# Kernel optimization log

Hardware: AMD Instinct MI355X
Metric: run time of the kernel (lower is better)

Reference implementation:

```python
import jax, jax.numpy as jnp
import numpy as np

B, S, D, H, DFF = 4, 2048, 1024, 16, 4096
HD = D // H  # head_dim = 64


def rmsnorm(x, scale, eps=1e-6):
    var = jnp.mean(jnp.square(x), axis=-1, keepdims=True)
    return x * jax.lax.rsqrt(var + eps) * scale


def setup_inputs() -> dict:
    key = jax.random.key(0)
    ks = jax.random.split(key, 16)
    s = 1.0 / np.sqrt(D)
    inp = {
        "x": jax.random.normal(ks[0], (B, S, D), jnp.float32),
        "wq": jax.random.normal(ks[1], (D, D), jnp.float32) * s,
        "bq": jnp.zeros((D,), jnp.float32),
        "wk": jax.random.normal(ks[2], (D, D), jnp.float32) * s,
        "bk": jnp.zeros((D,), jnp.float32),
        "wv": jax.random.normal(ks[3], (D, D), jnp.float32) * s,
        "bv": jnp.zeros((D,), jnp.float32),
        "wbeta": jax.random.normal(ks[4], (D, H), jnp.float32) * s,
        "bbeta": jnp.zeros((H,), jnp.float32),
        "wo": jax.random.normal(ks[5], (D, D), jnp.float32) * s,
        "bo": jnp.zeros((D,), jnp.float32),
        "w1": jax.random.normal(ks[6], (D, DFF), jnp.float32) * s,
        "b1": jnp.zeros((DFF,), jnp.float32),
        "w2": jax.random.normal(ks[7], (DFF, D), jnp.float32) * (1.0 / np.sqrt(DFF)),
        "b2": jnp.zeros((D,), jnp.float32),
        "ln1_scale": jnp.ones((D,), jnp.float32),
        "ln2_scale": jnp.ones((D,), jnp.float32),
    }
    return inp


def gdn_attention(x, wq, bq, wk, bk, wv, bv, wbeta, bbeta, wo, bo):
    b, s, _ = x.shape
    q = (x @ wq + bq).reshape(b, s, H, HD)
    k = (x @ wk + bk).reshape(b, s, H, HD)
    v = (x @ wv + bv).reshape(b, s, H, HD)
    k = k / (jnp.linalg.norm(k, axis=-1, keepdims=True) + 1e-6)
    beta = jax.nn.sigmoid(x @ wbeta + bbeta)[..., None]  # (b, s, H, 1)

    # time-major for scan: (s, b, H, ...)
    q = jnp.transpose(q, (1, 0, 2, 3))
    k = jnp.transpose(k, (1, 0, 2, 3))
    v = jnp.transpose(v, (1, 0, 2, 3))
    beta = jnp.transpose(beta, (1, 0, 2, 3))

    def _step(Sm, inputs):
        q_t, k_t, v_t, beta_t = inputs
        Sk = jnp.einsum('bhde,bhe->bhd', Sm, k_t)
        delta = v_t - Sk
        Sm = Sm + beta_t[..., None] * jnp.einsum('bhd,bhe->bhde', delta, k_t)
        o_t = jnp.einsum('bhde,bhe->bhd', Sm, q_t)
        return Sm, o_t

    S0 = jnp.zeros((b, H, HD, HD), x.dtype)
    _, outputs = jax.lax.scan(_step, S0, (q, k, v, beta))
    outputs = jnp.transpose(outputs, (1, 0, 2, 3)).reshape(b, s, D)
    return outputs @ wo + bo


def reference(x, wq, bq, wk, bk, wv, bv, wbeta, bbeta, wo, bo,
              w1, b1, w2, b2, ln1_scale, ln2_scale):
    residual = x
    h = rmsnorm(x, ln1_scale)
    h = gdn_attention(h, wq, bq, wk, bk, wv, bv, wbeta, bbeta, wo, bo)
    x = h + residual
    residual = x
    h = rmsnorm(x, ln2_scale)
    h = jax.nn.gelu(h @ w1 + b1) @ w2 + b2
    return h + residual
```

## Files before the change

### kernel.cpp

```cpp
#include <hip/hip_runtime.h>

#define DEV __device__ __forceinline__

typedef short bf16x8 __attribute__((ext_vector_type(8)));
typedef float f32x4 __attribute__((ext_vector_type(4)));
typedef unsigned int uint;

#define SBAR()   asm volatile("s_barrier" ::: "memory")
#define WAITV(n) asm volatile("s_waitcnt vmcnt(" #n ")" ::: "memory")
#define WAITL()  asm volatile("s_waitcnt lgkmcnt(0)" ::: "memory")

DEV unsigned short f2b(float f) {
    uint u = __float_as_uint(f);
    u += 0x7fffu + ((u >> 16) & 1u);
    return (unsigned short)(u >> 16);
}
DEV uint packbf2(float a, float b) { return (uint)f2b(a) | ((uint)f2b(b) << 16); }
DEV float b2f(unsigned short s) { return __uint_as_float(((uint)s) << 16); }
DEV float b2f_lo(uint u) { return __uint_as_float(u << 16); }
DEV float b2f_hi(uint u) { return __uint_as_float(u & 0xffff0000u); }

DEV void async_cp16(const void* g, void* l) {
    __builtin_amdgcn_global_load_lds(
        (const __attribute__((address_space(1))) unsigned int*)g,
        (__attribute__((address_space(3))) unsigned int*)l, 16, 0, 0);
}

DEV float quad_sum(float x) {
    x += __int_as_float(__builtin_amdgcn_update_dpp(0, __float_as_int(x), 0xB1, 0xF, 0xF, true));
    x += __int_as_float(__builtin_amdgcn_update_dpp(0, __float_as_int(x), 0x4E, 0xF, 0xF, true));
    return x;
}

DEV float gelu_f(float u) {
    float p = u + 0.044715f * u * u * u;
    float e = __expf(-1.5957691216f * p);
    return __fdividef(u, 1.f + e);
}

DEV void dec8(uint4 p, float* o) {
    o[0] = b2f_lo(p.x); o[1] = b2f_hi(p.x); o[2] = b2f_lo(p.y); o[3] = b2f_hi(p.y);
    o[4] = b2f_lo(p.z); o[5] = b2f_hi(p.z); o[6] = b2f_lo(p.w); o[7] = b2f_hi(p.w);
}

__global__ __launch_bounds__(256) void weight_prep_k(
    const float* __restrict__ wq, const float* __restrict__ wk,
    const float* __restrict__ wv, const float* __restrict__ wbeta,
    const float* __restrict__ wo, const float* __restrict__ w1,
    const float* __restrict__ w2,
    unsigned short* __restrict__ wqkvT, unsigned short* __restrict__ woT,
    unsigned short* __restrict__ w1T, unsigned short* __restrict__ w2T,
    const float* __restrict__ bq, const float* __restrict__ bk,
    const float* __restrict__ bv, const float* __restrict__ bb,
    float* __restrict__ biasc)
{
    const int id = blockIdx.x;
    if (id >= 12544) {
        int i = (id - 12544) * 256 + threadIdx.x;
        if (i >= 3328) return;
        float v = 0.f;
        if (i < 1024)      v = bq[i];
        else if (i < 2048) v = bk[i - 1024];
        else if (i < 3072) v = bv[i - 2048];
        else if (i < 3088) v = bb[i - 3072];
        biasc[i] = v;
        return;
    }
    const float* in; unsigned short* out; int K, N, KT, loc;
    if (id < 1024)      { in = wq;    out = wqkvT;               K = 1024; N = 1024; KT = 32;  loc = id; }
    else if (id < 2048) { in = wk;    out = wqkvT + 1024 * 1024; K = 1024; N = 1024; KT = 32;  loc = id - 1024; }
    else if (id < 3072) { in = wv;    out = wqkvT + 2048 * 1024; K = 1024; N = 1024; KT = 32;  loc = id - 2048; }
    else if (id < 3328) { in = wbeta; out = wqkvT + 3072 * 1024; K = 1024; N = 16;   KT = 32;  loc = id - 3072; }
    else if (id < 4352) { in = wo;    out = woT;                 K = 1024; N = 1024; KT = 32;  loc = id - 3328; }
    else if (id < 8448) { in = w1;    out = w1T;                 K = 1024; N = 4096; KT = 32;  loc = id - 4352; }
    else                { in = w2;    out = w2T;                 K = 4096; N = 1024; KT = 128; loc = id - 8448; }
    const int k0 = (loc % KT) * 32, n0 = (loc / KT) * 32;

    __shared__ float tile[32][33];
    const int tx = threadIdx.x & 31, ty = threadIdx.x >> 5;
#pragma unroll
    for (int i = 0; i < 32; i += 8) {
        int n = n0 + tx;
        tile[ty + i][tx] = (n < N) ? in[(size_t)(k0 + ty + i) * N + n] : 0.0f;
    }
    __syncthreads();
#pragma unroll
    for (int i = 0; i < 32; i += 8) {
        out[(size_t)(n0 + ty + i) * K + (k0 + tx)] = f2b(tile[tx][ty + i]);
    }
}

__global__ __launch_bounds__(256) void rmsnorm_cast_k(
    const float* __restrict__ x, const float* __restrict__ scale,
    unsigned short* __restrict__ out)
{
    const int row = blockIdx.x;
    const int t = threadIdx.x;
    const float4 v = *(const float4*)(x + (size_t)row * 1024 + t * 4);
    float ss = v.x * v.x + v.y * v.y + v.z * v.z + v.w * v.w;
#pragma unroll
    for (int off = 1; off < 64; off <<= 1) ss += __shfl_xor(ss, off);
    __shared__ float wsum[4];
    if ((t & 63) == 0) wsum[t >> 6] = ss;
    __syncthreads();
    const float tot = wsum[0] + wsum[1] + wsum[2] + wsum[3];
    const float inv = rsqrtf(tot * (1.0f / 1024.0f) + 1e-6f);
    const float4 sc = *(const float4*)(scale + t * 4);
    uint lo = (uint)f2b(v.x * inv * sc.x) | ((uint)f2b(v.y * inv * sc.y) << 16);
    uint hi = (uint)f2b(v.z * inv * sc.z) | ((uint)f2b(v.w * inv * sc.w) << 16);
    uint2 pkd; pkd.x = lo; pkd.y = hi;
    *(uint2*)(out + (size_t)row * 1024 + t * 4) = pkd;
}

template <bool GELU, bool GUARD>
__global__ __launch_bounds__(512, 2) void gemm256(
    const unsigned short* __restrict__ A, const unsigned short* __restrict__ BT,
    const float* __restrict__ bias, unsigned short* __restrict__ C,
    int Nstride, int Nreal, int K)
{
    __shared__ __align__(16) unsigned short As[4][256 * 32];
    __shared__ __align__(16) unsigned short Bs[4][256 * 32];
    const int tid = threadIdx.x;
    const int wid = tid >> 6;
    const int lane = tid & 63;
    const int l16 = lane & 15, quad = lane >> 4;
    const int wm = wid & 1, wn = wid >> 1;
    const int m0 = blockIdx.x << 8, n0 = blockIdx.y << 8;

    const int srow = (wid << 5) + (lane >> 2);
    const int scol = ((lane & 3) ^ ((lane >> 3) & 3)) << 3;
    const unsigned short* Ag = A + (size_t)(m0 + srow) * K + scol;
    const unsigned short* Bg = BT + (size_t)(n0 + srow) * K + scol;
    const size_t rstep16 = (size_t)16 * K;
    const int ldst = wid << 10;

    f32x4 acc[8][4];
#pragma unroll
    for (int i = 0; i < 8; i++)
#pragma unroll
        for (int j = 0; j < 4; j++) acc[i][j] = (f32x4)0.f;

    const int ksw = (quad ^ ((l16 >> 1) & 3)) << 3;
    const int aoff = ((wm << 7) + l16) * 32 + ksw;
    const int boff = ((wn << 6) + l16) * 32 + ksw;

    const int nt = K >> 5;
    async_cp16(Ag, &As[0][ldst]);
    async_cp16(Ag + rstep16, &As[0][ldst + 512]);
    async_cp16(Bg, &Bs[0][ldst]);
    async_cp16(Bg + rstep16, &Bs[0][ldst + 512]);
    async_cp16(Ag + 32, &As[1][ldst]);
    async_cp16(Ag + 32 + rstep16, &As[1][ldst + 512]);
    async_cp16(Bg + 32, &Bs[1][ldst]);
    async_cp16(Bg + 32 + rstep16, &Bs[1][ldst + 512]);
    WAITV(4);
    SBAR();

    for (int tb = 0; tb < nt; tb += 4) {
#pragma unroll
        for (int u = 0; u < 4; ++u) {
            const int t = tb + u;
            const int pb = (u + 2) & 3;
            const bool st = (t + 2) < nt;
            const size_t kpre = (size_t)(t + 2) << 5;
            bf16x8 af[8], bfr[4];
#pragma unroll
            for (int mi = 0; mi < 8; mi++) af[mi] = *(const bf16x8*)&As[u][aoff + mi * 512];
#pragma unroll
            for (int ni = 0; ni < 4; ni++) bfr[ni] = *(const bf16x8*)&Bs[u][boff + ni * 512];
            if (st) {
                async_cp16(Ag + kpre, &As[pb][ldst]);
                async_cp16(Ag + kpre + rstep16, &As[pb][ldst + 512]);
                async_cp16(Bg + kpre, &Bs[pb][ldst]);
                async_cp16(Bg + kpre + rstep16, &Bs[pb][ldst + 512]);
                WAITV(4);
            } else {
                WAITV(0);
            }
            SBAR();
            __builtin_amdgcn_s_setprio(1);
#pragma unroll
            for (int mi = 0; mi < 8; mi++)
#pragma unroll
                for (int ni = 0; ni < 4; ni++)
                    acc[mi][ni] = __builtin_amdgcn_mfma_f32_16x16x32_bf16(af[mi], bfr[ni], acc[mi][ni], 0, 0, 0);
            __builtin_amdgcn_s_setprio(0);
            SBAR();
        }
    }

    float bv[4];
    const int ccol = n0 + (wn << 6) + l16;
#pragma unroll
    for (int ni = 0; ni < 4; ni++) bv[ni] = bias[ccol + ni * 16];
#pragma unroll
    for (int mi = 0; mi < 8; mi++) {
        const int row = m0 + (wm << 7) + mi * 16 + (quad << 2);
#pragma unroll
        for (int r = 0; r < 4; r++) {
            unsigned short* Crow = C + (size_t)(row + r) * Nstride + ccol;
#pragma unroll
            for (int ni = 0; ni < 4; ni++) {
                float v = acc[mi][ni][r] + bv[ni];
                if (GELU) v = gelu_f(v);
                if (!GUARD || (ccol + ni * 16) < Nreal) Crow[ni * 16] = f2b(v);
            }
        }
    }
}

template <bool ADD>
__global__ __launch_bounds__(512, 2) void gemm128n256(
    const unsigned short* __restrict__ A, const unsigned short* __restrict__ BT,
    const float* __restrict__ bias, const float* __restrict__ add,
    float* __restrict__ C, int N, int K)
{
    __shared__ __align__(16) unsigned short As[4][128 * 32];
    __shared__ __align__(16) unsigned short Bs[4][256 * 32];
    const int tid = threadIdx.x;
    const int wid = tid >> 6;
    const int lane = tid & 63;
    const int l16 = lane & 15, quad = lane >> 4;
    const int wm = wid & 1, wn = wid >> 1;
    const int m0 = blockIdx.x << 7, n0 = blockIdx.y << 8;

    const int arow = (wid << 4) + (lane >> 2);
    const int brow = (wid << 5) + (lane >> 2);
    const int scol = ((lane & 3) ^ ((lane >> 3) & 3)) << 3;
    const unsigned short* Ag = A + (size_t)(m0 + arow) * K + scol;
    const unsigned short* Bg = BT + (size_t)(n0 + brow) * K + scol;
    const size_t rstep16 = (size_t)16 * K;
    const int lda = wid << 9;
    const int ldb = wid << 10;

    f32x4 acc[4][4];
#pragma unroll
    for (int i = 0; i < 4; i++)
#pragma unroll
        for (int j = 0; j < 4; j++) acc[i][j] = (f32x4)0.f;

    const int ksw = (quad ^ ((l16 >> 1) & 3)) << 3;
    const int aoff = ((wm << 6) + l16) * 32 + ksw;
    const int boff = ((wn << 6) + l16) * 32 + ksw;

    const int nt = K >> 5;
    async_cp16(Ag, &As[0][lda]);
    async_cp16(Bg, &Bs[0][ldb]);
    async_cp16(Bg + rstep16, &Bs[0][ldb + 512]);
    async_cp16(Ag + 32, &As[1][lda]);
    async_cp16(Bg + 32, &Bs[1][ldb]);
    async_cp16(Bg + 32 + rstep16, &Bs[1][ldb + 512]);
    WAITV(3);
    SBAR();

    for (int tb = 0; tb < nt; tb += 4) {
#pragma unroll
        for (int u = 0; u < 4; ++u) {
            const int t = tb + u;
            const int pb = (u + 2) & 3;
            const bool st = (t + 2) < nt;
            const size_t kpre = (size_t)(t + 2) << 5;
            bf16x8 af[4], bfr[4];
#pragma unroll
            for (int mi = 0; mi < 4; mi++) af[mi] = *(const bf16x8*)&As[u][aoff + mi * 512];
#pragma unroll
            for (int ni = 0; ni < 4; ni++) bfr[ni] = *(const bf16x8*)&Bs[u][boff + ni * 512];
            if (st) {
                async_cp16(Ag + kpre, &As[pb][lda]);
                async_cp16(Bg + kpre, &Bs[pb][ldb]);
                async_cp16(Bg + kpre + rstep16, &Bs[pb][ldb + 512]);
                WAITV(3);
            } else {
                WAITV(0);
            }
            SBAR();
            __builtin_amdgcn_s_setprio(1);
#pragma unroll
            for (int mi = 0; mi < 4; mi++)
#pragma unroll
                for (int ni = 0; ni < 4; ni++)
                    acc[mi][ni] = __builtin_amdgcn_mfma_f32_16x16x32_bf16(af[mi], bfr[ni], acc[mi][ni], 0, 0, 0);
            __builtin_amdgcn_s_setprio(0);
            SBAR();
        }
    }

    const int ccol = n0 + (wn << 6) + l16;
    float bv[4];
#pragma unroll
    for (int ni = 0; ni < 4; ni++) bv[ni] = bias[ccol + ni * 16];
#pragma unroll
    for (int mi = 0; mi < 4; mi++) {
        const int row = m0 + (wm << 6) + mi * 16 + (quad << 2);
#pragma unroll
        for (int r = 0; r < 4; r++) {
#pragma unroll
            for (int ni = 0; ni < 4; ni++) {
                size_t idx = (size_t)(row + r) * N + ccol + ni * 16;
                float v = acc[mi][ni][r] + bv[ni];
                if (ADD) v += add[idx];
                C[idx] = v;
            }
        }
    }
}


__global__ __launch_bounds__(256) void gdn_prep(
    unsigned short* __restrict__ qkv, unsigned short* __restrict__ Wg,
    unsigned short* __restrict__ ZTg, unsigned short* __restrict__ KTg)
{
    const int chunk = blockIdx.x, bh = blockIdx.y;
    const int b = bh >> 4, h = bh & 15;
    __shared__ float Ks[64 * 68];
    __shared__ float Ws[64 * 65];
    __shared__ float Zs[64 * 65];
    __shared__ float Asl[64 * 65];
    __shared__ float bs[64];
    const int tid = threadIdx.x;
    const int t = tid >> 2, c = tid & 3;
    unsigned short* rowp = qkv + (size_t)(b * 2048 + chunk * 64 + t) * 3200;

    float kn[16];
    {
        uint4 ka = *(const uint4*)(rowp + 1024 + h * 64 + 16 * c);
        uint4 kb = *(const uint4*)(rowp + 1024 + h * 64 + 16 * c + 8);
        dec8(ka, kn); dec8(kb, kn + 8);
    }
    float ss = 0.f;
#pragma unroll
    for (int j = 0; j < 16; j++) ss += kn[j] * kn[j];
    ss = quad_sum(ss);
    const float inv = 1.f / (sqrtf(ss) + 1e-6f);
#pragma unroll
    for (int j = 0; j < 16; j++) kn[j] *= inv;
#pragma unroll
    for (int j = 0; j < 16; j++) Ks[t * 68 + 16 * c + j] = kn[j];
    {
        uint4 p0, p1;
        p0.x = packbf2(kn[0], kn[1]);  p0.y = packbf2(kn[2], kn[3]);
        p0.z = packbf2(kn[4], kn[5]);  p0.w = packbf2(kn[6], kn[7]);
        p1.x = packbf2(kn[8], kn[9]);  p1.y = packbf2(kn[10], kn[11]);
        p1.z = packbf2(kn[12], kn[13]); p1.w = packbf2(kn[14], kn[15]);
        *(uint4*)(rowp + 1024 + h * 64 + 16 * c) = p0;
        *(uint4*)(rowp + 1024 + h * 64 + 16 * c + 8) = p1;
    }
    if (c == 0) bs[t] = 1.f / (1.f + __expf(-b2f(rowp[3072 + h])));
    __syncthreads();

    const float beta = bs[t];
#pragma unroll
    for (int j = 0; j < 16; j++) Ws[t * 65 + 16 * c + j] = beta * kn[j];
    {
        float vv[16];
        uint4 va = *(const uint4*)(rowp + 2048 + h * 64 + 16 * c);
        uint4 vb = *(const uint4*)(rowp + 2048 + h * 64 + 16 * c + 8);
        dec8(va, vv); dec8(vb, vv + 8);
#pragma unroll
        for (int j = 0; j < 16; j++) Zs[t * 65 + 16 * c + j] = beta * vv[j];
    }
    __syncthreads();

    {
        const int tt = tid >> 4, sx = tid & 15;
        float dm[4][4];
#pragma unroll
        for (int i = 0; i < 4; i++)
#pragma unroll
            for (int j = 0; j < 4; j++) dm[i][j] = 0.f;
        for (int d = 0; d < 64; d++) {
            float kt[4], ksv[4];
#pragma unroll
            for (int i = 0; i < 4; i++) kt[i] = Ks[(4 * tt + i) * 68 + d];
#pragma unroll
            for (int j = 0; j < 4; j++) ksv[j] = Ks[(4 * sx + j) * 68 + d];
#pragma unroll
            for (int i = 0; i < 4; i++)
#pragma unroll
                for (int j = 0; j < 4; j++) dm[i][j] += kt[i] * ksv[j];
        }
#pragma unroll
        for (int i = 0; i < 4; i++)
#pragma unroll
            for (int j = 0; j < 4; j++) {
                int T = 4 * tt + i, S_ = 4 * sx + j;
                Asl[T * 65 + S_] = (S_ < T) ? bs[T] * dm[i][j] : 0.f;
            }
    }
    __syncthreads();

    {
        const int wid = tid >> 6, lane = tid & 63;
        for (int qi = 0; qi < 4; qi++) {
            if (qi > 0) {
                const int tb = qi * 16 + wid * 4;
                float aw[4], az[4];
#pragma unroll
                for (int i = 0; i < 4; i++) { aw[i] = Ws[(tb + i) * 65 + lane]; az[i] = Zs[(tb + i) * 65 + lane]; }
                for (int s = 0; s < qi * 16; s++) {
                    float wsv = Ws[s * 65 + lane], zsv = Zs[s * 65 + lane];
#pragma unroll
                    for (int i = 0; i < 4; i++) {
                        float a = Asl[(tb + i) * 65 + s];
                        aw[i] -= a * wsv; az[i] -= a * zsv;
                    }
                }
#pragma unroll
                for (int i = 0; i < 4; i++) { Ws[(tb + i) * 65 + lane] = aw[i]; Zs[(tb + i) * 65 + lane] = az[i]; }
            }
            __syncthreads();
            if (wid == 0) {
                for (int T = qi * 16; T < qi * 16 + 16; T++) {
                    float a_ = Ws[T * 65 + lane];
                    for (int s = qi * 16; s < T; s++) a_ -= Asl[T * 65 + s] * Ws[s * 65 + lane];
                    Ws[T * 65 + lane] = a_;
                }
            } else if (wid == 1) {
                for (int T = qi * 16; T < qi * 16 + 16; T++) {
                    float a_ = Zs[T * 65 + lane];
                    for (int s = qi * 16; s < T; s++) a_ -= Asl[T * 65 + s] * Zs[s * 65 + lane];
                    Zs[T * 65 + lane] = a_;
                }
            }
            __syncthreads();
        }
    }

    const size_t cbase = ((size_t)bh * 32 + chunk) * 4096;
    {
#pragma unroll
        for (int half = 0; half < 2; half++) {
            uint4 w4;
            w4.x = packbf2(Ws[t * 65 + 16 * c + half * 8 + 0], Ws[t * 65 + 16 * c + half * 8 + 1]);
            w4.y = packbf2(Ws[t * 65 + 16 * c + half * 8 + 2], Ws[t * 65 + 16 * c + half * 8 + 3]);
            w4.z = packbf2(Ws[t * 65 + 16 * c + half * 8 + 4], Ws[t * 65 + 16 * c + half * 8 + 5]);
            w4.w = packbf2(Ws[t * 65 + 16 * c + half * 8 + 6], Ws[t * 65 + 16 * c + half * 8 + 7]);
            *(uint4*)(Wg + cbase + (size_t)((2 * c + half) * 64 + t) * 8) = w4;
        }
    }
    {
        const int jj = tid >> 2, tq = tid & 3;
#pragma unroll
        for (int half = 0; half < 2; half++) {
            uint4 z4;
            int i0 = half * 8;
            z4.x = packbf2(Zs[(16 * tq + i0 + 0) * 65 + jj], Zs[(16 * tq + i0 + 1) * 65 + jj]);
            z4.y = packbf2(Zs[(16 * tq + i0 + 2) * 65 + jj], Zs[(16 * tq + i0 + 3) * 65 + jj]);
            z4.z = packbf2(Zs[(16 * tq + i0 + 4) * 65 + jj], Zs[(16 * tq + i0 + 5) * 65 + jj]);
            z4.w = packbf2(Zs[(16 * tq + i0 + 6) * 65 + jj], Zs[(16 * tq + i0 + 7) * 65 + jj]);
            *(uint4*)(ZTg + cbase + (size_t)((2 * tq + half) * 64 + jj) * 8) = z4;
        }
    }
    {
        const int dd = tid >> 2, tq = tid & 3;
#pragma unroll
        for (int half = 0; half < 2; half++) {
            uint4 k4;
            int i0 = half * 8;
            k4.x = packbf2(Ks[(16 * tq + i0 + 0) * 68 + dd], Ks[(16 * tq + i0 + 1) * 68 + dd]);
            k4.y = packbf2(Ks[(16 * tq + i0 + 2) * 68 + dd], Ks[(16 * tq + i0 + 3) * 68 + dd]);
            k4.z = packbf2(Ks[(16 * tq + i0 + 4) * 68 + dd], Ks[(16 * tq + i0 + 5) * 68 + dd]);
            k4.w = packbf2(Ks[(16 * tq + i0 + 6) * 68 + dd], Ks[(16 * tq + i0 + 7) * 68 + dd]);
            *(uint4*)(KTg + cbase + (size_t)((2 * tq + half) * 64 + dd) * 8) = k4;
        }
    }
}

__global__ __launch_bounds__(64, 1) void gdn_prop_mfma(
    const unsigned short* __restrict__ Wg, const unsigned short* __restrict__ KTg,
    const unsigned short* __restrict__ ZTg, unsigned short* __restrict__ Sg,
    unsigned short* __restrict__ YTg)
{
    const int bh = blockIdx.x;
    const int jb = blockIdx.y << 4;
    __shared__ unsigned short Wb[2][4096];
    __shared__ unsigned short KTb[2][4096];
    __shared__ unsigned short ZTb[2][1024];
    __shared__ unsigned short Sb[1024];
    const int lane = threadIdx.x;
    const int l16 = lane & 15, quad = lane >> 4;

    f32x4 Sacc[4];
#pragma unroll
    for (int dt = 0; dt < 4; dt++) Sacc[dt] = (f32x4)0.f;

    {
        const size_t cb0 = ((size_t)bh * 32) * 4096;
#pragma unroll
        for (int p = 0; p < 8; p++) async_cp16(Wg + cb0 + p * 512 + lane * 8, &Wb[0][p * 512]);
#pragma unroll
        for (int p = 0; p < 8; p++) async_cp16(KTg + cb0 + p * 512 + lane * 8, &KTb[0][p * 512]);
#pragma unroll
        for (int c = 0; c < 2; c++)
            async_cp16(ZTg + cb0 + (size_t)((c * 4 + (lane >> 4)) * 64 + jb + (lane & 15)) * 8,
                       &ZTb[0][c * 512]);
    }
    WAITV(0);

    for (int ch = 0; ch < 32; ch++) {
        const int cur = ch & 1, nxt = cur ^ 1;
        const size_t cbase = ((size_t)bh * 32 + ch) * 4096;

        if (ch + 1 < 32) {
            const size_t cbn = cbase + 4096;
#pragma unroll
            for (int p = 0; p < 8; p++) async_cp16(Wg + cbn + p * 512 + lane * 8, &Wb[nxt][p * 512]);
#pragma unroll
            for (int p = 0; p < 8; p++) async_cp16(KTg + cbn + p * 512 + lane * 8, &KTb[nxt][p * 512]);
#pragma unroll
            for (int c = 0; c < 2; c++)
                async_cp16(ZTg + cbn + (size_t)((c * 4 + (lane >> 4)) * 64 + jb + (lane & 15)) * 8,
                           &ZTb[nxt][c * 512]);
        }

#pragma unroll
        for (int dt = 0; dt < 4; dt++) {
#pragma unroll
            for (int r = 0; r < 4; r++) {
                const int lj = quad * 4 + r;
                Sb[((2 * dt + (l16 >> 3)) * 16 + lj) * 8 + (l16 & 7)] = f2b(Sacc[dt][r]);
            }
        }
        {
            const int gd = lane >> 3, lj0 = (lane & 7) * 2;
            uint4 s0 = *(const uint4*)&Sb[lane * 16];
            uint4 s1 = *(const uint4*)&Sb[lane * 16 + 8];
            *(uint4*)(Sg + cbase + (size_t)(gd * 64 + jb + lj0) * 8) = s0;
            *(uint4*)(Sg + cbase + (size_t)(gd * 64 + jb + lj0 + 1) * 8) = s1;
        }

        f32x4 t1[4];
#pragma unroll
        for (int tt = 0; tt < 4; tt++) t1[tt] = (f32x4)0.f;
#pragma unroll
        for (int kh = 0; kh < 2; kh++) {
            const int g = kh * 4 + quad;
            bf16x8 afr = *(const bf16x8*)&Sb[(g * 16 + l16) * 8];
#pragma unroll
            for (int tt = 0; tt < 4; tt++) {
                bf16x8 bfr = *(const bf16x8*)&Wb[cur][(g * 64 + tt * 16 + l16) * 8];
                t1[tt] = __builtin_amdgcn_mfma_f32_16x16x32_bf16(afr, bfr, t1[tt], 0, 0, 0);
            }
        }
#pragma unroll
        for (int tt = 0; tt < 4; tt++) {
            const int t = tt * 16 + l16;
            unsigned short ybf[4];
#pragma unroll
            for (int r = 0; r < 4; r++) {
                const int lj = quad * 4 + r;
                const float z = b2f(ZTb[cur][((t >> 3) * 16 + lj) * 8 + (t & 7)]);
                ybf[r] = f2b(z - t1[tt][r]);
            }
#pragma unroll
            for (int r = 0; r < 4; r++) {
                const int lj = quad * 4 + r;
                ZTb[cur][((t >> 3) * 16 + lj) * 8 + (t & 7)] = ybf[r];
            }
        }
#pragma unroll
        for (int kh = 0; kh < 2; kh++) {
            const int g = kh * 4 + quad;
            bf16x8 afr = *(const bf16x8*)&ZTb[cur][(g * 16 + l16) * 8];
#pragma unroll
            for (int dt = 0; dt < 4; dt++) {
                bf16x8 bfr = *(const bf16x8*)&KTb[cur][(g * 64 + dt * 16 + l16) * 8];
                Sacc[dt] = __builtin_amdgcn_mfma_f32_16x16x32_bf16(afr, bfr, Sacc[dt], 0, 0, 0);
            }
        }
        {
            const int gt = lane >> 3, lj0 = (lane & 7) * 2;
            uint4 y0 = *(const uint4*)&ZTb[cur][lane * 16];
            uint4 y1 = *(const uint4*)&ZTb[cur][lane * 16 + 8];
            *(uint4*)(YTg + cbase + (size_t)(gt * 64 + jb + lj0) * 8) = y0;
            *(uint4*)(YTg + cbase + (size_t)(gt * 64 + jb + lj0 + 1) * 8) = y1;
        }
        WAITV(0);
    }
}

__global__ __launch_bounds__(256) void gdn_out(
    const unsigned short* __restrict__ qkv, const unsigned short* __restrict__ YTg,
    const unsigned short* __restrict__ Sg, unsigned short* __restrict__ attn)
{
    const int chunk = blockIdx.x, bh = blockIdx.y;
    const int b = bh >> 4, h = bh & 15;
    __shared__ unsigned short QbU[8 * 516];
    __shared__ unsigned short KbU[8 * 516];
    __shared__ unsigned short StU[8 * 516];
    __shared__ unsigned short YtU[8 * 516];
    __shared__ unsigned short MhU[8 * 516];
    __shared__ unsigned short MlU[8 * 516];
    const int tid = threadIdx.x;
    const int wid = tid >> 6, lane = tid & 63;
    const int l16 = lane & 15, quad = lane >> 4;
    const size_t cbase = ((size_t)bh * 32 + chunk) * 4096;

    {
        const int t = tid >> 2, c = tid & 3;
        const unsigned short* rowp = qkv + (size_t)(b * 2048 + chunk * 64 + t) * 3200;
        uint4 qa = *(const uint4*)(rowp + h * 64 + 16 * c);
        uint4 qb = *(const uint4*)(rowp + h * 64 + 16 * c + 8);
        uint4 ka = *(const uint4*)(rowp + 1024 + h * 64 + 16 * c);
        uint4 kb = *(const uint4*)(rowp + 1024 + h * 64 + 16 * c + 8);
        *(uint4*)&QbU[(2 * c) * 516 + t * 8]     = qa;
        *(uint4*)&QbU[(2 * c + 1) * 516 + t * 8] = qb;
        *(uint4*)&KbU[(2 * c) * 516 + t * 8]     = ka;
        *(uint4*)&KbU[(2 * c + 1) * 516 + t * 8] = kb;
        const int g = tid >> 5, row = (tid * 2) & 63;
        uint4 s0 = *(const uint4*)(Sg + cbase + tid * 16);
        uint4 s1 = *(const uint4*)(Sg + cbase + tid * 16 + 8);
        *(uint4*)&StU[g * 516 + row * 8]       = s0;
        *(uint4*)&StU[g * 516 + (row + 1) * 8] = s1;
        uint4 y0 = *(const uint4*)(YTg + cbase + tid * 16);
        uint4 y1 = *(const uint4*)(YTg + cbase + tid * 16 + 8);
        *(uint4*)&YtU[g * 516 + row * 8]       = y0;
        *(uint4*)&YtU[g * 516 + (row + 1) * 8] = y1;
    }
    __syncthreads();

    f32x4 m[4], o[4];
#pragma unroll
    for (int i = 0; i < 4; i++) { m[i] = (f32x4)0.f; o[i] = (f32x4)0.f; }

#pragma unroll
    for (int kh = 0; kh < 2; kh++) {
        const int g = kh * 4 + quad;
        bf16x8 afr = *(const bf16x8*)&QbU[g * 516 + (wid * 16 + l16) * 8];
#pragma unroll
        for (int st = 0; st < 4; st++) {
            bf16x8 bk = *(const bf16x8*)&KbU[g * 516 + (st * 16 + l16) * 8];
            m[st] = __builtin_amdgcn_mfma_f32_16x16x32_bf16(afr, bk, m[st], 0, 0, 0);
        }
#pragma unroll
        for (int jt = 0; jt < 4; jt++) {
            bf16x8 bs_ = *(const bf16x8*)&StU[g * 516 + (jt * 16 + l16) * 8];
            o[jt] = __builtin_amdgcn_mfma_f32_16x16x32_bf16(afr, bs_, o[jt], 0, 0, 0);
        }
    }

#pragma unroll
    for (int st = 0; st < 4; st++) {
#pragma unroll
        for (int r = 0; r < 4; r++) {
            const int t = wid * 16 + quad * 4 + r;
            const int s = st * 16 + l16;
            float v = (s <= t) ? m[st][r] : 0.f;
            unsigned short hi = f2b(v);
            unsigned short lo = f2b(v - b2f(hi));
            const int addr = (s >> 3) * 516 + t * 8 + (s & 7);
            MhU[addr] = hi;
            MlU[addr] = lo;
        }
    }
    __syncthreads();

#pragma unroll
    for (int kh = 0; kh < 2; kh++) {
        const int g = kh * 4 + quad;
        bf16x8 ah = *(const bf16x8*)&MhU[g * 516 + (wid * 16 + l16) * 8];
        bf16x8 al = *(const bf16x8*)&MlU[g * 516 + (wid * 16 + l16) * 8];
#pragma unroll
        for (int jt = 0; jt < 4; jt++) {
            bf16x8 by = *(const bf16x8*)&YtU[g * 516 + (jt * 16 + l16) * 8];
            o[jt] = __builtin_amdgcn_mfma_f32_16x16x32_bf16(ah, by, o[jt], 0, 0, 0);
            o[jt] = __builtin_amdgcn_mfma_f32_16x16x32_bf16(al, by, o[jt], 0, 0, 0);
        }
    }

#pragma unroll
    for (int jt = 0; jt < 4; jt++) {
#pragma unroll
        for (int r = 0; r < 4; r++) {
            const int t = wid * 16 + quad * 4 + r;
            attn[(size_t)(b * 2048 + chunk * 64 + t) * 1024 + h * 64 + jt * 16 + l16] = f2b(o[jt][r]);
        }
    }
}

static constexpr size_t OFF_H     = 0;
static constexpr size_t OFF_WQKVT = OFF_H + 16777216;
static constexpr size_t OFF_WOT   = OFF_WQKVT + 6553600;
static constexpr size_t OFF_W1T   = OFF_WOT + 2097152;
static constexpr size_t OFF_W2T   = OFF_W1T + 8388608;
static constexpr size_t OFF_BIAS  = OFF_W2T + 8388608;
static constexpr size_t OFF_QKV   = OFF_BIAS + 16384;
static constexpr size_t OFF_ATTN  = OFF_QKV + 67108864;
static constexpr size_t OFF_Y1    = OFF_ATTN + 16777216;
static constexpr size_t OFF_WG    = OFF_Y1 + 33554432;
static constexpr size_t OFF_YG    = OFF_WG + 16777216;

extern "C" void kernel_launch(void* const* d_in, const int* in_sizes, int n_in,
                              void* d_out, int out_size, void* d_ws, size_t ws_size,
                              hipStream_t stream)
{
    const float* x     = (const float*)d_in[0];
    const float* wq    = (const float*)d_in[1];
    const float* bq    = (const float*)d_in[2];
    const float* wk    = (const float*)d_in[3];
    const float* bk    = (const float*)d_in[4];
    const float* wv    = (const float*)d_in[5];
    const float* bv    = (const float*)d_in[6];
    const float* wbeta = (const float*)d_in[7];
    const float* bbeta = (const float*)d_in[8];
    const float* wo    = (const float*)d_in[9];
    const float* bo    = (const float*)d_in[10];
    const float* w1    = (const float*)d_in[11];
    const float* b1    = (const float*)d_in[12];
    const float* w2    = (const float*)d_in[13];
    const float* b2    = (const float*)d_in[14];
    const float* ln1   = (const float*)d_in[15];
    const float* ln2   = (const float*)d_in[16];

    char* ws = (char*)d_ws;
    unsigned short* hbuf  = (unsigned short*)(ws + OFF_H);
    unsigned short* Sg    = (unsigned short*)(ws + OFF_H);
    unsigned short* wqkvT = (unsigned short*)(ws + OFF_WG);
    unsigned short* woT   = (unsigned short*)(ws + OFF_WOT);
    unsigned short* w1T   = (unsigned short*)(ws + OFF_W1T);
    unsigned short* w2T   = (unsigned short*)(ws + OFF_W2T);
    float*          biasc = (float*)(ws + OFF_BIAS);
    unsigned short* qkvU  = (unsigned short*)(ws + OFF_QKV);
    unsigned short* gbuf  = (unsigned short*)(ws + OFF_QKV);
    unsigned short* attn  = (unsigned short*)(ws + OFF_ATTN);
    float*          y1    = (float*)(ws + OFF_Y1);
    unsigned short* ZTg   = (unsigned short*)(ws + OFF_Y1);
    unsigned short* KTg   = (unsigned short*)(ws + OFF_Y1 + 16777216);
    unsigned short* Wg    = (unsigned short*)(ws + OFF_WG);
    unsigned short* YTg   = (unsigned short*)(ws + OFF_YG);
    float*          out   = (float*)d_out;

    weight_prep_k<<<12557, 256, 0, stream>>>(wq, wk, wv, wbeta, wo, w1, w2,
                                             wqkvT, woT, w1T, w2T,
                                             bq, bk, bv, bbeta, biasc);

    rmsnorm_cast_k<<<8192, 256, 0, stream>>>(x, ln1, hbuf);
    gemm256<false, true><<<dim3(32, 13), 512, 0, stream>>>(hbuf, wqkvT, biasc, qkvU, 3200, 3200, 1024);
    gdn_prep<<<dim3(32, 64), 256, 0, stream>>>(qkvU, Wg, ZTg, KTg);
    gdn_prop_mfma<<<dim3(64, 4), 64, 0, stream>>>(Wg, KTg, ZTg, Sg, YTg);
    gdn_out<<<dim3(32, 64), 256, 0, stream>>>(qkvU, YTg, Sg, attn);
    gemm128n256<true><<<dim3(64, 4), 512, 0, stream>>>(attn, woT, bo, x, y1, 1024, 1024);
    rmsnorm_cast_k<<<8192, 256, 0, stream>>>(y1, ln2, hbuf);
    gemm256<true, false><<<dim3(32, 16), 512, 0, stream>>>(hbuf, w1T, b1, gbuf, 4096, 4096, 1024);
    gemm128n256<true><<<dim3(64, 4), 512, 0, stream>>>(gbuf, w2T, b2, y1, out, 1024, 4096);
}
```

Baseline: 576.2 us.

## Restructure gemm256 to BK=64 double-buffered pipeline and use MFMA for chunk K·Kᵀ

The main 256x256 GEMM moves from four 32-wide K stages to two 64-wide K buffers. It interleaves A-fragment loads, async global-to-LDS staging and MFMA phases inside each iteration, and uses a new 8-way XOR swizzle. This is meant to cut barriers per K element and hide load latency better. In gdn_prep, the scalar FP32 64x64 K·Kᵀ product is replaced by bf16 MFMA from a transposed bf16 copy of K kept in LDS, which lowers precision on the strictly lower-triangular A matrix. The second GEMM's shared arrays are only renamed.

```diff
diff --git a/kernel.cpp b/kernel.cpp
--- a/kernel.cpp
+++ b/kernel.cpp
@@ -112,14 +112,44 @@
     *(uint2*)(out + (size_t)row * 1024 + t * 4) = pkd;
 }
 
+#define STG(dst, srcp, half, kt)                                                       \
+    do {                                                                               \
+        async_cp16(srcp + (size_t)((half) * 128) * K + ((kt) << 6),                    \
+                   dst + ((half) * 128) * 64 + lds);                                   \
+        async_cp16(srcp + (size_t)((half) * 128 + 64) * K + ((kt) << 6),               \
+                   dst + ((half) * 128 + 64) * 64 + lds);                              \
+    } while (0)
+
+#define LD_A(MI0)                                                                      \
+    do {                                                                               \
+        af[0] = *(const bf16x8*)&Ab[arow0 + (MI0) * 1024 + k0];                        \
+        af[1] = *(const bf16x8*)&Ab[arow0 + (MI0) * 1024 + k1];                        \
+        af[2] = *(const bf16x8*)&Ab[arow0 + ((MI0) + 1) * 1024 + k0];                  \
+        af[3] = *(const bf16x8*)&Ab[arow0 + ((MI0) + 1) * 1024 + k1];                  \
+    } while (0)
+
+#define PH_MFMA(MI0)                                                                   \
+    do {                                                                               \
+        __builtin_amdgcn_s_setprio(1);                                                 \
+        _Pragma("unroll")                                                              \
+        for (int kh = 0; kh < 2; kh++)                                                 \
+            _Pragma("unroll")                                                          \
+            for (int m = 0; m < 2; m++)                                                \
+                _Pragma("unroll")                                                      \
+                for (int ni = 0; ni < 4; ni++)                                         \
+                    acc[(MI0) + m][ni] = __builtin_amdgcn_mfma_f32_16x16x32_bf16(      \
+                        af[m * 2 + kh], bf[ni * 2 + kh], acc[(MI0) + m][ni], 0, 0, 0); \
+        __builtin_amdgcn_s_setprio(0);                                                 \
+    } while (0)
+
 template <bool GELU, bool GUARD>
 __global__ __launch_bounds__(512, 2) void gemm256(
     const unsigned short* __restrict__ A, const unsigned short* __restrict__ BT,
     const float* __restrict__ bias, unsigned short* __restrict__ C,
     int Nstride, int Nreal, int K)
 {
-    __shared__ __align__(16) unsigned short As[4][256 * 32];
-    __shared__ __align__(16) unsigned short Bs[4][256 * 32];
+    __shared__ __align__(16) unsigned short As[2][256 * 64];
+    __shared__ __align__(16) unsigned short Bs[2][256 * 64];
     const int tid = threadIdx.x;
     const int wid = tid >> 6;
     const int lane = tid & 63;
@@ -127,12 +157,11 @@
     const int wm = wid & 1, wn = wid >> 1;
     const int m0 = blockIdx.x << 8, n0 = blockIdx.y << 8;
 
-    const int srow = (wid << 5) + (lane >> 2);
-    const int scol = ((lane & 3) ^ ((lane >> 3) & 3)) << 3;
+    const int srow = (wid << 3) + (lane >> 3);
+    const int scol = ((lane & 7) ^ ((lane >> 3) & 7)) << 3;
     const unsigned short* Ag = A + (size_t)(m0 + srow) * K + scol;
     const unsigned short* Bg = BT + (size_t)(n0 + srow) * K + scol;
-    const size_t rstep16 = (size_t)16 * K;
-    const int ldst = wid << 10;
+    const int lds = (wid << 3) * 64;
 
     f32x4 acc[8][4];
 #pragma unroll
@@ -140,53 +169,43 @@
 #pragma unroll
         for (int j = 0; j < 4; j++) acc[i][j] = (f32x4)0.f;
 
-    const int ksw = (quad ^ ((l16 >> 1) & 3)) << 3;
-    const int aoff = ((wm << 7) + l16) * 32 + ksw;
-    const int boff = ((wn << 6) + l16) * 32 + ksw;
-
-    const int nt = K >> 5;
-    async_cp16(Ag, &As[0][ldst]);
-    async_cp16(Ag + rstep16, &As[0][ldst + 512]);
-    async_cp16(Bg, &Bs[0][ldst]);
-    async_cp16(Bg + rstep16, &Bs[0][ldst + 512]);
-    async_cp16(Ag + 32, &As[1][ldst]);
-    async_cp16(Ag + 32 + rstep16, &As[1][ldst + 512]);
-    async_cp16(Bg + 32, &Bs[1][ldst]);
-    async_cp16(Bg + 32 + rstep16, &Bs[1][ldst + 512]);
-    WAITV(4);
-    SBAR();
-
-    for (int tb = 0; tb < nt; tb += 4) {
-#pragma unroll
-        for (int u = 0; u < 4; ++u) {
-            const int t = tb + u;
-            const int pb = (u + 2) & 3;
-            const bool st = (t + 2) < nt;
-            const size_t kpre = (size_t)(t + 2) << 5;
-            bf16x8 af[8], bfr[4];
-#pragma unroll
-            for (int mi = 0; mi < 8; mi++) af[mi] = *(const bf16x8*)&As[u][aoff + mi * 512];
-#pragma unroll
-            for (int ni = 0; ni < 4; ni++) bfr[ni] = *(const bf16x8*)&Bs[u][boff + ni * 512];
-            if (st) {
-                async_cp16(Ag + kpre, &As[pb][ldst]);
-                async_cp16(Ag + kpre + rstep16, &As[pb][ldst + 512]);
-                async_cp16(Bg + kpre, &Bs[pb][ldst]);
-                async_cp16(Bg + kpre + rstep16, &Bs[pb][ldst + 512]);
-                WAITV(4);
-            } else {
-                WAITV(0);
-            }
-            SBAR();
-            __builtin_amdgcn_s_setprio(1);
-#pragma unroll
-            for (int mi = 0; mi < 8; mi++)
-#pragma unroll
-                for (int ni = 0; ni < 4; ni++)
-                    acc[mi][ni] = __builtin_amdgcn_mfma_f32_16x16x32_bf16(af[mi], bfr[ni], acc[mi][ni], 0, 0, 0);
-            __builtin_amdgcn_s_setprio(0);
-            SBAR();
-        }
+    const int arow0 = ((wm << 7) + l16) << 6;
+    const int brow0 = ((wn << 6) + l16) << 6;
+    const int k0 = (quad ^ (l16 & 7)) << 3;
+    const int k1 = k0 ^ 32;
+
+    const int nt = K >> 6;
+    STG(Bs[0], Bg, 0, 0); STG(Bs[0], Bg, 1, 0);
+    STG(As[0], Ag, 0, 0); STG(As[0], Ag, 1, 0);
+    STG(Bs[1], Bg, 0, 1); STG(Bs[1], Bg, 1, 1);
+
+    for (int t = 0; t < nt; ++t) {
+        const unsigned short* Ab = As[t & 1];
+        const unsigned short* Bb = Bs[t & 1];
+        unsigned short* An = As[(t + 1) & 1];
+        unsigned short* Bn = Bs[t & 1];
+        const bool s1 = (t + 1) < nt, s2 = (t + 2) < nt;
+        if (s2) { WAITV(4); } else { WAITV(0); }
+        SBAR();
+        bf16x8 af[4], bf[8];
+#pragma unroll
+        for (int ni = 0; ni < 4; ni++) {
+            bf[ni * 2]     = *(const bf16x8*)&Bb[brow0 + ni * 1024 + k0];
+            bf[ni * 2 + 1] = *(const bf16x8*)&Bb[brow0 + ni * 1024 + k1];
+        }
+        LD_A(0);
+        if (s1) { STG(An, Ag, 0, t + 1); }
+        PH_MFMA(0);
+        LD_A(2);
+        if (s1) { STG(An, Ag, 1, t + 1); }
+        PH_MFMA(2);
+        SBAR();
+        LD_A(4);
+        if (s2) { STG(Bn, Bg, 0, t + 2); }
+        PH_MFMA(4);
+        LD_A(6);
+        if (s2) { STG(Bn, Bg, 1, t + 2); }
+        PH_MFMA(6);
     }
 
     float bv[4];
@@ -215,8 +234,8 @@
     const float* __restrict__ bias, const float* __restrict__ add,
     float* __restrict__ C, int N, int K)
 {
-    __shared__ __align__(16) unsigned short As[4][128 * 32];
-    __shared__ __align__(16) unsigned short Bs[4][256 * 32];
+    __shared__ __align__(16) unsigned short As2[4][128 * 32];
+    __shared__ __align__(16) unsigned short Bs2[4][256 * 32];
     const int tid = threadIdx.x;
     const int wid = tid >> 6;
     const int lane = tid & 63;
@@ -244,12 +263,12 @@
     const int boff = ((wn << 6) + l16) * 32 + ksw;
 
     const int nt = K >> 5;
-    async_cp16(Ag, &As[0][lda]);
-    async_cp16(Bg, &Bs[0][ldb]);
-    async_cp16(Bg + rstep16, &Bs[0][ldb + 512]);
-    async_cp16(Ag + 32, &As[1][lda]);
-    async_cp16(Bg + 32, &Bs[1][ldb]);
-    async_cp16(Bg + 32 + rstep16, &Bs[1][ldb + 512]);
+    async_cp16(Ag, &As2[0][lda]);
+    async_cp16(Bg, &Bs2[0][ldb]);
+    async_cp16(Bg + rstep16, &Bs2[0][ldb + 512]);
+    async_cp16(Ag + 32, &As2[1][lda]);
+    async_cp16(Bg + 32, &Bs2[1][ldb]);
+    async_cp16(Bg + 32 + rstep16, &Bs2[1][ldb + 512]);
     WAITV(3);
     SBAR();
 
@@ -262,13 +281,13 @@
             const size_t kpre = (size_t)(t + 2) << 5;
             bf16x8 af[4], bfr[4];
 #pragma unroll
-            for (int mi = 0; mi < 4; mi++) af[mi] = *(const bf16x8*)&As[u][aoff + mi * 512];
-#pragma unroll
-            for (int ni = 0; ni < 4; ni++) bfr[ni] = *(const bf16x8*)&Bs[u][boff + ni * 512];
+            for (int mi = 0; mi < 4; mi++) af[mi] = *(const bf16x8*)&As2[u][aoff + mi * 512];
+#pragma unroll
+            for (int ni = 0; ni < 4; ni++) bfr[ni] = *(const bf16x8*)&Bs2[u][boff + ni * 512];
             if (st) {
-                async_cp16(Ag + kpre, &As[pb][lda]);
-                async_cp16(Bg + kpre, &Bs[pb][ldb]);
-                async_cp16(Bg + kpre + rstep16, &Bs[pb][ldb + 512]);
+                async_cp16(Ag + kpre, &As2[pb][lda]);
+                async_cp16(Bg + kpre, &Bs2[pb][ldb]);
+                async_cp16(Bg + kpre + rstep16, &Bs2[pb][ldb + 512]);
                 WAITV(3);
             } else {
                 WAITV(0);
@@ -317,6 +336,7 @@
     __shared__ float Zs[64 * 65];
     __shared__ float Asl[64 * 65];
     __shared__ float bs[64];
+    __shared__ __align__(16) unsigned short KTb[4096];
     const int tid = threadIdx.x;
     const int t = tid >> 2, c = tid & 3;
     unsigned short* rowp = qkv + (size_t)(b * 2048 + chunk * 64 + t) * 3200;
@@ -344,6 +364,8 @@
         p1.z = packbf2(kn[12], kn[13]); p1.w = packbf2(kn[14], kn[15]);
         *(uint4*)(rowp + 1024 + h * 64 + 16 * c) = p0;
         *(uint4*)(rowp + 1024 + h * 64 + 16 * c + 8) = p1;
+        *(uint4*)&KTb[((2 * c) * 64 + t) * 8]     = p0;
+        *(uint4*)&KTb[((2 * c + 1) * 64 + t) * 8] = p1;
     }
     if (c == 0) bs[t] = 1.f / (1.f + __expf(-b2f(rowp[3072 + h])));
     __syncthreads();
@@ -362,29 +384,28 @@
     __syncthreads();
 
     {
-        const int tt = tid >> 4, sx = tid & 15;
-        float dm[4][4];
-#pragma unroll
-        for (int i = 0; i < 4; i++)
-#pragma unroll
-            for (int j = 0; j < 4; j++) dm[i][j] = 0.f;
-        for (int d = 0; d < 64; d++) {
-            float kt[4], ksv[4];
-#pragma unroll
-            for (int i = 0; i < 4; i++) kt[i] = Ks[(4 * tt + i) * 68 + d];
-#pragma unroll
-            for (int j = 0; j < 4; j++) ksv[j] = Ks[(4 * sx + j) * 68 + d];
-#pragma unroll
-            for (int i = 0; i < 4; i++)
-#pragma unroll
-                for (int j = 0; j < 4; j++) dm[i][j] += kt[i] * ksv[j];
-        }
-#pragma unroll
-        for (int i = 0; i < 4; i++)
-#pragma unroll
-            for (int j = 0; j < 4; j++) {
-                int T = 4 * tt + i, S_ = 4 * sx + j;
-                Asl[T * 65 + S_] = (S_ < T) ? bs[T] * dm[i][j] : 0.f;
+        const int wid2 = tid >> 6, lane2 = tid & 63;
+        const int l16 = lane2 & 15, quad = lane2 >> 4;
+        f32x4 am[4];
+#pragma unroll
+        for (int st = 0; st < 4; st++) am[st] = (f32x4)0.f;
+#pragma unroll
+        for (int kh = 0; kh < 2; kh++) {
+            const int g = kh * 4 + quad;
+            bf16x8 afr = *(const bf16x8*)&KTb[(g * 64 + wid2 * 16 + l16) * 8];
+#pragma unroll
+            for (int st = 0; st < 4; st++) {
+                bf16x8 bfr = *(const bf16x8*)&KTb[(g * 64 + st * 16 + l16) * 8];
+                am[st] = __builtin_amdgcn_mfma_f32_16x16x32_bf16(afr, bfr, am[st], 0, 0, 0);
+            }
+        }
+#pragma unroll
+        for (int st = 0; st < 4; st++)
+#pragma unroll
+            for (int r = 0; r < 4; r++) {
+                const int T = wid2 * 16 + quad * 4 + r;
+                const int S_ = st * 16 + l16;
+                Asl[T * 65 + S_] = (S_ < T) ? bs[T] * am[st][r] : 0.f;
             }
     }
     __syncthreads();
```

After: 552.2 us. -4.2%, faster.
